# Performance work log

Measured on AMD Instinct MI355X. Metric: run time of the kernel, lower is better.

## Reference

```python
import jax, jax.numpy as jnp
import numpy as np

NUM_HEADS = 64
HEAD_DIM = 8

def setup_inputs() -> dict:
    key = jax.random.key(0)
    k1, k2, k3, k4, k5 = jax.random.split(key, 5)
    s = 0.02
    return {
        'x': jax.random.normal(k1, (4, 8192, 2048), dtype=jnp.float32),
        'w_qkv': jax.random.normal(k2, (768, 2048), dtype=jnp.float32) * s,
        'w_z': jax.random.normal(k3, (512, 2048), dtype=jnp.float32) * s,
        'w_b': jax.random.normal(k4, (64, 2048), dtype=jnp.float32) * s,
        'w_a': jax.random.normal(k5, (64, 2048), dtype=jnp.float32) * s,
    }

def reference(x, w_qkv, w_z, w_b, w_a):
    B, S, _ = x.shape
    qkv = jnp.einsum('bsh,dh->bsd', x, w_qkv)                     # [B,S,768]
    z = jnp.einsum('bsh,dh->bsd', x, w_z)                          # [B,S,512]
    z = z.reshape(B, S, NUM_HEADS, HEAD_DIM)
    b = jax.nn.sigmoid(jnp.einsum('bsh,dh->bsd', x, w_b))          # [B,S,64]
    a = jnp.einsum('bsh,dh->bsd', x, w_a) * b                      # [B,S,64]
    out = (qkv.sum(-1, keepdims=True)
           + z.sum(-1).sum(-1, keepdims=True)
           + a.sum(-1, keepdims=True))                             # [B,S,1]
    return out
```

## Files before the change

kernel.cpp:

```cpp
#include <hip/hip_runtime.h>
#include <stdint.h>

using bf16x8_t = __attribute__((ext_vector_type(8))) __bf16;
using f32x4_t  = __attribute__((ext_vector_type(4))) float;
using u16x8_t  = __attribute__((ext_vector_type(8))) unsigned short;

#define KD 2048

static __device__ __forceinline__ unsigned short f2bf(float f) {
  union { float f; unsigned u; } v; v.f = f;
  unsigned r = v.u + 0x7fffu + ((v.u >> 16) & 1u);
  return (unsigned short)(r >> 16);
}

__global__ void k_prep(const float* __restrict__ wqkv, const float* __restrict__ wz,
                       const float* __restrict__ wb, const float* __restrict__ wa,
                       unsigned short* __restrict__ wbf3) {
  __shared__ float red[4][8];
  const int b = blockIdx.x, t = threadIdx.x;
  if (b < 128) {
    const int u = b * 256 + t;
    const int l = u & 63;
    const int vv = u >> 6;
    const int nf = vv & 7;
    const int s  = vv >> 3;
    const int k  = s * 32 + ((l >> 4) << 3);
    const int c  = nf * 16 + (l & 15);
    const float* src = (c < 64) ? (wa + (size_t)c * KD + k)
                                : (wb + (size_t)(c - 64) * KD + k);
    f32x4_t v0 = *(const f32x4_t*)(src);
    f32x4_t v1 = *(const f32x4_t*)(src + 4);
    u16x8_t o;
    o[0]=f2bf(v0[0]); o[1]=f2bf(v0[1]); o[2]=f2bf(v0[2]); o[3]=f2bf(v0[3]);
    o[4]=f2bf(v1[0]); o[5]=f2bf(v1[1]); o[6]=f2bf(v1[2]); o[7]=f2bf(v1[3]);
    *(u16x8_t*)(wbf3 + (size_t)((s * 9 + nf) * 64 + l) * 8) = o;
  } else if (b < 384) {
    const int bw = b - 128;
    const int c = t & 7;
    const int rg = t >> 3;
    const int h = bw * 8 + c;
    float s = 0.f;
    #pragma unroll 8
    for (int i = 0; i < 40; ++i) {
      const int r = rg + 32 * i;
      const float* p = (r < 768) ? (wqkv + (size_t)r * KD)
                                 : (wz + (size_t)(r - 768) * KD);
      s += p[h];
    }
    s += __shfl_xor(s, 8, 64);
    s += __shfl_xor(s, 16, 64);
    s += __shfl_xor(s, 32, 64);
    const int lane = t & 63, wv = t >> 6;
    if (lane < 8) red[wv][lane] = s;
    __syncthreads();
    if (t < 8) {
      const float val = red[0][t] + red[1][t] + red[2][t] + red[3][t];
      const int hh = bw * 8 + t;
      const int s9 = hh >> 5;
      const int g  = (hh & 31) >> 3;
      const int j  = hh & 7;
      wbf3[(size_t)((s9 * 9 + 8) * 64 + (g << 4)) * 8 + j] = f2bf(val);
    }
  } else {
    const int idx = (b - 384) * 256 + t;
    const int s = idx >> 6, l = idx & 63;
    if (l & 15) {
      u16x8_t z; z[0]=0;z[1]=0;z[2]=0;z[3]=0;z[4]=0;z[5]=0;z[6]=0;z[7]=0;
      *(u16x8_t*)(wbf3 + (size_t)((s * 9 + 8) * 64 + l) * 8) = z;
    }
  }
}

__global__ __launch_bounds__(512, 1) void k_main(
    const float* __restrict__ x, const unsigned short* __restrict__ wbf3,
    float* __restrict__ out)
{
  __shared__ __align__(16) unsigned char lds[135168];
  const int t = threadIdx.x;
  const int lane = t & 63;
  const int wv = t >> 6;
  const int g = lane >> 4;
  const int r15 = lane & 15;
  const size_t tile = (size_t)blockIdx.x * 128;

  f32x4_t acc[9];
  #pragma unroll
  for (int i = 0; i < 9; ++i) acc[i] = f32x4_t{0.f, 0.f, 0.f, 0.f};

  auto STAGE_W = [&](int it) {
    unsigned char* wbp = lds + 98304 + (it & 1) * 18432;
    const unsigned short* gw = wbf3 + (size_t)it * 9216 + lane * 8;
    __builtin_amdgcn_global_load_lds(
        (const __attribute__((address_space(1))) void*)(gw + wv * 512),
        (__attribute__((address_space(3))) void*)(wbp + wv * 1024), 16, 0, 0);
    __builtin_amdgcn_global_load_lds(
        (const __attribute__((address_space(1))) void*)(gw + (wv + 8) * 512),
        (__attribute__((address_space(3))) void*)(wbp + (wv + 8) * 1024), 16, 0, 0);
    if (wv < 2)
      __builtin_amdgcn_global_load_lds(
          (const __attribute__((address_space(1))) void*)(gw + (16 + wv) * 512),
          (__attribute__((address_space(3))) void*)(wbp + (16 + wv) * 1024), 16, 0, 0);
  };
  auto STAGE_X = [&](int it, int bsel) {
    unsigned char* xbp = lds + bsel * 32768;
    #pragma unroll
    for (int i = 0; i < 4; ++i) {
      const int ch = wv * 4 + i;
      const int r = ch * 4 + (lane >> 4);
      const int c = (lane & 15) ^ (r & 15);
      const float* src = x + (tile + r) * KD + it * 64 + c * 4;
      __builtin_amdgcn_global_load_lds(
          (const __attribute__((address_space(1))) void*)src,
          (__attribute__((address_space(3))) void*)(xbp + ch * 1024), 16, 0, 0);
    }
  };
  auto COMPUTE = [&](int it, int xbsel) {
    const unsigned char* xbp = lds + xbsel * 32768;
    const unsigned char* wbp = lds + 98304 + (it & 1) * 18432;
    const int r = wv * 16 + r15;
    const unsigned char* xr = xbp + r * 256;
    #pragma unroll
    for (int kh = 0; kh < 2; ++kh) {
      const int c0 = kh * 8 + g * 2;
      f32x4_t lo = *(const f32x4_t*)(xr + ((c0       ^ r15) * 16));
      f32x4_t hi = *(const f32x4_t*)(xr + (((c0 + 1) ^ r15) * 16));
      bf16x8_t af;
      af[0] = (__bf16)lo[0]; af[1] = (__bf16)lo[1];
      af[2] = (__bf16)lo[2]; af[3] = (__bf16)lo[3];
      af[4] = (__bf16)hi[0]; af[5] = (__bf16)hi[1];
      af[6] = (__bf16)hi[2]; af[7] = (__bf16)hi[3];
      #pragma unroll
      for (int nf = 0; nf < 9; ++nf) {
        bf16x8_t bfr = *(const bf16x8_t*)(wbp + ((kh * 9 + nf) * 64 + lane) * 16);
        acc[nf] = __builtin_amdgcn_mfma_f32_16x16x32_bf16(af, bfr, acc[nf], 0, 0, 0);
      }
    }
  };

  STAGE_W(0);
  STAGE_X(0, 0);
  STAGE_X(1, 1);

  int xb = 0;
  for (int it = 0; it < 31; ++it) {
    asm volatile("s_waitcnt vmcnt(4)" ::: "memory");
    __builtin_amdgcn_s_barrier();
    __builtin_amdgcn_sched_barrier(0);
    STAGE_W(it + 1);
    if (it < 30) {
      int b2 = xb + 2; if (b2 >= 3) b2 -= 3;
      STAGE_X(it + 2, b2);
    }
    COMPUTE(it, xb);
    ++xb; if (xb == 3) xb = 0;
  }
  asm volatile("s_waitcnt vmcnt(0)" ::: "memory");
  __builtin_amdgcn_s_barrier();
  __builtin_amdgcn_sched_barrier(0);
  COMPUTE(31, xb);

  #pragma unroll
  for (int r = 0; r < 4; ++r) {
    float v = 0.f;
    #pragma unroll
    for (int nf = 0; nf < 4; ++nf) {
      float av = acc[nf][r];
      float bv = acc[nf + 4][r];
      v += av / (1.f + __expf(-bv));
    }
    v += __shfl_xor(v, 1, 64);
    v += __shfl_xor(v, 2, 64);
    v += __shfl_xor(v, 4, 64);
    v += __shfl_xor(v, 8, 64);
    if (r15 == 0) out[tile + wv * 16 + g * 4 + r] = v + acc[8][r];
  }
}

extern "C" void kernel_launch(void* const* d_in, const int* in_sizes, int n_in,
                              void* d_out, int out_size, void* d_ws, size_t ws_size,
                              hipStream_t stream) {
  const float* x    = (const float*)d_in[0];
  const float* wqkv = (const float*)d_in[1];
  const float* wz   = (const float*)d_in[2];
  const float* wb   = (const float*)d_in[3];
  const float* wa   = (const float*)d_in[4];
  float* out = (float*)d_out;

  unsigned short* wbf3 = (unsigned short*)d_ws;

  k_prep<<<400, 256, 0, stream>>>(wqkv, wz, wb, wa, wbf3);
  k_main<<<out_size / 128, 512, 0, stream>>>(x, wbf3, out);
}
```

Before: 54.92 us.

## Fuse weight prep and main GEMM into one cooperative kernel with grid sync

Merges the weight-conversion/column-sum prep kernel into the main kernel. Every block first does a slice of the prep work, using LDS for the partial reduction. A grid-wide cooperative sync then makes the prepared bf16 weights visible before the MFMA main loop starts. The goal is to remove the separate kernel launch and the inter-kernel gap. In exchange it adds a grid barrier and relies on all 256 single-occupancy blocks being co-resident.

After: 143.5 us. +161.2%, slower.

```diff
diff --git a/kernel.cpp b/kernel.cpp
--- a/kernel.cpp
+++ b/kernel.cpp
@@ -1,5 +1,8 @@
 #include <hip/hip_runtime.h>
+#include <hip/hip_cooperative_groups.h>
 #include <stdint.h>
+
+namespace cg = cooperative_groups;
 
 using bf16x8_t = __attribute__((ext_vector_type(8))) __bf16;
 using f32x4_t  = __attribute__((ext_vector_type(4))) float;
@@ -13,71 +16,77 @@
   return (unsigned short)(r >> 16);
 }
 
-__global__ void k_prep(const float* __restrict__ wqkv, const float* __restrict__ wz,
-                       const float* __restrict__ wb, const float* __restrict__ wa,
-                       unsigned short* __restrict__ wbf3) {
-  __shared__ float red[4][8];
-  const int b = blockIdx.x, t = threadIdx.x;
-  if (b < 128) {
-    const int u = b * 256 + t;
-    const int l = u & 63;
-    const int vv = u >> 6;
-    const int nf = vv & 7;
-    const int s  = vv >> 3;
-    const int k  = s * 32 + ((l >> 4) << 3);
-    const int c  = nf * 16 + (l & 15);
-    const float* src = (c < 64) ? (wa + (size_t)c * KD + k)
-                                : (wb + (size_t)(c - 64) * KD + k);
-    f32x4_t v0 = *(const f32x4_t*)(src);
-    f32x4_t v1 = *(const f32x4_t*)(src + 4);
-    u16x8_t o;
-    o[0]=f2bf(v0[0]); o[1]=f2bf(v0[1]); o[2]=f2bf(v0[2]); o[3]=f2bf(v0[3]);
-    o[4]=f2bf(v1[0]); o[5]=f2bf(v1[1]); o[6]=f2bf(v1[2]); o[7]=f2bf(v1[3]);
-    *(u16x8_t*)(wbf3 + (size_t)((s * 9 + nf) * 64 + l) * 8) = o;
-  } else if (b < 384) {
-    const int bw = b - 128;
-    const int c = t & 7;
-    const int rg = t >> 3;
-    const int h = bw * 8 + c;
-    float s = 0.f;
-    #pragma unroll 8
-    for (int i = 0; i < 40; ++i) {
-      const int r = rg + 32 * i;
-      const float* p = (r < 768) ? (wqkv + (size_t)r * KD)
-                                 : (wz + (size_t)(r - 768) * KD);
-      s += p[h];
-    }
-    s += __shfl_xor(s, 8, 64);
-    s += __shfl_xor(s, 16, 64);
-    s += __shfl_xor(s, 32, 64);
-    const int lane = t & 63, wv = t >> 6;
-    if (lane < 8) red[wv][lane] = s;
-    __syncthreads();
-    if (t < 8) {
-      const float val = red[0][t] + red[1][t] + red[2][t] + red[3][t];
-      const int hh = bw * 8 + t;
-      const int s9 = hh >> 5;
-      const int g  = (hh & 31) >> 3;
-      const int j  = hh & 7;
-      wbf3[(size_t)((s9 * 9 + 8) * 64 + (g << 4)) * 8 + j] = f2bf(val);
-    }
-  } else {
-    const int idx = (b - 384) * 256 + t;
-    const int s = idx >> 6, l = idx & 63;
-    if (l & 15) {
-      u16x8_t z; z[0]=0;z[1]=0;z[2]=0;z[3]=0;z[4]=0;z[5]=0;z[6]=0;z[7]=0;
-      *(u16x8_t*)(wbf3 + (size_t)((s * 9 + 8) * 64 + l) * 8) = z;
-    }
-  }
-}
-
-__global__ __launch_bounds__(512, 1) void k_main(
-    const float* __restrict__ x, const unsigned short* __restrict__ wbf3,
+__global__ __launch_bounds__(512, 1) void k_fused(
+    const float* __restrict__ x, const float* __restrict__ wqkv,
+    const float* __restrict__ wz, const float* __restrict__ wb,
+    const float* __restrict__ wa, unsigned short* __restrict__ wbf3,
     float* __restrict__ out)
 {
   __shared__ __align__(16) unsigned char lds[135168];
   const int t = threadIdx.x;
   const int lane = t & 63;
+
+  {
+    const int gid = blockIdx.x * 512 + t;
+    const bool ws_role = (gid >= 32768) && (gid < 98304);
+    float sv = 0.f;
+    if (gid < 32768) {
+      const int u = gid;
+      const int l = u & 63;
+      const int vv = u >> 6;
+      const int nf = vv & 7;
+      const int s  = vv >> 3;
+      const int k  = s * 32 + ((l >> 4) << 3);
+      const int c  = nf * 16 + (l & 15);
+      const float* src = (c < 64) ? (wa + (size_t)c * KD + k)
+                                  : (wb + (size_t)(c - 64) * KD + k);
+      f32x4_t v0 = *(const f32x4_t*)(src);
+      f32x4_t v1 = *(const f32x4_t*)(src + 4);
+      u16x8_t o;
+      o[0]=f2bf(v0[0]); o[1]=f2bf(v0[1]); o[2]=f2bf(v0[2]); o[3]=f2bf(v0[3]);
+      o[4]=f2bf(v1[0]); o[5]=f2bf(v1[1]); o[6]=f2bf(v1[2]); o[7]=f2bf(v1[3]);
+      *(u16x8_t*)(wbf3 + (size_t)((s * 9 + nf) * 64 + l) * 8) = o;
+    } else if (ws_role) {
+      const int u2 = gid - 32768;
+      const int tt = u2 & 255;
+      const int c8 = tt & 7;
+      const int rg = tt >> 3;
+      const int h  = ((u2 >> 8) << 3) + c8;
+      #pragma unroll 8
+      for (int i = 0; i < 40; ++i) {
+        const int r = rg + 32 * i;
+        const float* p = (r < 768) ? (wqkv + (size_t)r * KD)
+                                   : (wz + (size_t)(r - 768) * KD);
+        sv += p[h];
+      }
+      sv += __shfl_xor(sv, 8, 64);
+      sv += __shfl_xor(sv, 16, 64);
+      sv += __shfl_xor(sv, 32, 64);
+      if (lane < 8)
+        ((float*)lds)[(t >> 8) * 32 + ((t >> 6) & 3) * 8 + lane] = sv;
+    } else if (gid < 102400) {
+      const int u3 = gid - 98304;
+      const int s = u3 >> 6, l = u3 & 63;
+      if (l & 15) {
+        u16x8_t z; z[0]=0;z[1]=0;z[2]=0;z[3]=0;z[4]=0;z[5]=0;z[6]=0;z[7]=0;
+        *(u16x8_t*)(wbf3 + (size_t)((s * 9 + 8) * 64 + l) * 8) = z;
+      }
+    }
+    __syncthreads();
+    if (ws_role && (t & 255) < 8) {
+      const float* red = (float*)lds + (t >> 8) * 32;
+      const float val = red[t & 7] + red[8 + (t & 7)] +
+                        red[16 + (t & 7)] + red[24 + (t & 7)];
+      const int hh = (((gid - 32768) >> 8) << 3) + (t & 7);
+      const int s9 = hh >> 5;
+      const int g  = (hh & 31) >> 3;
+      const int j  = hh & 7;
+      wbf3[(size_t)((s9 * 9 + 8) * 64 + (g << 4)) * 8 + j] = f2bf(val);
+    }
+  }
+  __threadfence();
+  cg::this_grid().sync();
+
   const int wv = t >> 6;
   const int g = lane >> 4;
   const int r15 = lane & 15;
@@ -188,6 +197,15 @@
 
   unsigned short* wbf3 = (unsigned short*)d_ws;
 
-  k_prep<<<400, 256, 0, stream>>>(wqkv, wz, wb, wa, wbf3);
-  k_main<<<out_size / 128, 512, 0, stream>>>(x, wbf3, out);
+  void* args[7];
+  args[0] = (void*)&x;
+  args[1] = (void*)&wqkv;
+  args[2] = (void*)&wz;
+  args[3] = (void*)&wb;
+  args[4] = (void*)&wa;
+  args[5] = (void*)&wbf3;
+  args[6] = (void*)&out;
+  hipLaunchCooperativeKernel((const void*)k_fused,
+                             dim3(out_size / 128), dim3(512),
+                             args, 0, stream);
 }
```
